# Kernel tuning notes

Hardware: AMD Instinct MI355X
Metric: run time of the kernel (lower is better)

Reference implementation:

```python
import jax, jax.numpy as jnp
import numpy as np

GRID_SIZE = 5
GRID_LO, GRID_HI = -1.0, 1.0


def setup_inputs() -> dict:
    key = jax.random.key(0)
    k1, k2 = jax.random.split(key)
    B, out_dim, in_dim, H, W = 8, 64, 64, 192, 192
    G = GRID_SIZE + 1
    x = jax.random.normal(k1, (B, in_dim, H, W), dtype=jnp.float32)
    coef = jax.random.normal(k2, (B, out_dim, in_dim, G), dtype=jnp.float32) * 0.1
    return {"x": x, "coef": coef}


def reference(x, coef):
    # x: [B, in_dim, H, W]; coef: [B, out_dim, in_dim, G] with G = grid_size + 1
    G = GRID_SIZE + 1
    grid = jnp.linspace(GRID_LO, GRID_HI, G, dtype=x.dtype)
    lo, hi = grid[0], grid[-1]
    spacing = grid[1] - grid[0]

    B, in_dim, H, W = x.shape
    out_dim = coef.shape[1]
    P = H * W

    xf = x.reshape(B, in_dim, P)
    xc = jnp.clip(xf, lo, hi)
    nx = (xc - lo) / spacing                      # normalized coordinate in [0, grid_size]
    idx = jnp.clip(jnp.floor(nx).astype(jnp.int32), 0, GRID_SIZE - 1)  # left knot
    frac = nx - idx.astype(x.dtype)               # fractional offset (grad flows via nx)
    w1 = 1.0 - frac
    w2 = frac
    idx_next = jnp.clip(idx + 1, 0, GRID_SIZE)    # right knot (max index = G-1)

    # Two-hot interpolation weights over the G grid points: [B, in, P, G]
    Wt = (w1[..., None] * jax.nn.one_hot(idx, G, dtype=x.dtype)
          + w2[..., None] * jax.nn.one_hot(idx_next, G, dtype=x.dtype))

    # result[b,o,p] = sum_i sum_g Wt[b,i,p,g] * coef[b,o,i,g]
    out = jnp.einsum('bipg,boig->bop', Wt, coef)
    return out.reshape(B, out_dim, H, W)
```

## Files before the change

kernel.cpp:

```cpp
#include <hip/hip_runtime.h>
#include <stdint.h>


typedef __fp16 half8_t __attribute__((ext_vector_type(8)));
typedef __fp16 half2_t __attribute__((ext_vector_type(2)));
typedef float f32x4 __attribute__((ext_vector_type(4)));

#define NBATCH 8
#define OD 64
#define ID 64
#define PIX 36864
#define NG 6
#define PT 192
#define KI 32
#define NCHUNK 2
#define KROW 384
#define PROW 196
#define PTILES (PIX / PT)

#define CPRE_BYTES (NBATCH * OD * KROW * 2)

__global__ __launch_bounds__(256)
void prep_coef(const float* __restrict__ coef, __fp16* __restrict__ cpre) {
  int idx = blockIdx.x * 256 + threadIdx.x;
  int b = idx / (OD * KROW);
  int rem = idx % (OD * KROW);
  int o = rem / KROW;
  int k = rem % KROW;
  int c = k / 192;
  int s = k % 192;
  int g = s >> 5;
  int iof = s & 31;
  float v = coef[((size_t)(b * OD + o) * ID + c * KI + iof) * NG + g];
  cpre[idx] = (__fp16)v;
}

__global__ __launch_bounds__(256, 3)
void kan_mfma2(const float* __restrict__ x, const __fp16* __restrict__ cpre,
               float* __restrict__ out) {
  const int t = threadIdx.x;
  const int lane = t & 63;
  const int wave = t >> 6;
  const int q8 = lane >> 4;
  const int col = lane & 15;

  const int bid = blockIdx.x;
  const int b = bid / PTILES;
  const int p0 = (bid % PTILES) * PT;

  __shared__ float nx_lds[KI][PROW] __attribute__((aligned(16)));

  f32x4 acc[4][3];
#pragma unroll
  for (int i = 0; i < 4; ++i)
#pragma unroll
    for (int j = 0; j < 3; ++j)
      acc[i][j] = (f32x4){0.f, 0.f, 0.f, 0.f};

  const float* xb = x + (size_t)b * ID * PIX + p0;
  const __fp16* caw = cpre + (size_t)b * OD * KROW + (size_t)col * KROW + q8 * 8;
  const int srow = t >> 3;
  const int pb = (t & 7) * 24;

  f32x4 xv[6];
#pragma unroll
  for (int j = 0; j < 6; ++j)
    xv[j] = *(const f32x4*)(xb + (size_t)srow * PIX + pb + 4 * j);

#pragma unroll
  for (int c = 0; c < NCHUNK; ++c) {
    if (c > 0) __syncthreads();

#pragma unroll
    for (int j = 0; j < 6; ++j) {
      f32x4 n;
#pragma unroll
      for (int r = 0; r < 4; ++r) {
        float v = fminf(fmaxf(xv[j][r], -1.f), 1.f);
        n[r] = (v + 1.f) * 2.5f;
      }
      *(f32x4*)&nx_lds[srow][pb + 4 * j] = n;
    }
    __syncthreads();

    if (c + 1 < NCHUNK) {
#pragma unroll
      for (int j = 0; j < 6; ++j)
        xv[j] = *(const f32x4*)(xb + (size_t)(KI + srow) * PIX + pb + 4 * j);
    }

    float nxv[3][8];
#pragma unroll
    for (int pti = 0; pti < 3; ++pti) {
      int p = wave * 48 + pti * 16 + col;
#pragma unroll
      for (int j = 0; j < 8; ++j)
        nxv[pti][j] = nx_lds[q8 * 8 + j][p];
    }

    const __fp16* cac = caw + c * 192;
#pragma unroll
    for (int ks = 0; ks < 6; ++ks) {
      half8_t af[4];
#pragma unroll
      for (int ot = 0; ot < 4; ++ot)
        af[ot] = *(const half8_t*)(cac + (size_t)(ot * 16) * KROW + ks * 32);

      const float gf = (float)ks;
#pragma unroll
      for (int pti = 0; pti < 3; ++pti) {
        union { half2_t h2[4]; half8_t v; } bu;
#pragma unroll
        for (int jj = 0; jj < 4; ++jj) {
          float h0 = fmaxf(0.f, 1.f - fabsf(nxv[pti][2 * jj] - gf));
          float h1 = fmaxf(0.f, 1.f - fabsf(nxv[pti][2 * jj + 1] - gf));
          bu.h2[jj] = __builtin_amdgcn_cvt_pkrtz(h0, h1);
        }
#pragma unroll
        for (int ot = 0; ot < 4; ++ot)
          acc[ot][pti] = __builtin_amdgcn_mfma_f32_16x16x32_f16(
              af[ot], bu.v, acc[ot][pti], 0, 0, 0);
      }
    }
  }

  float* ob = out + (size_t)b * OD * PIX + p0;
#pragma unroll
  for (int ot = 0; ot < 4; ++ot) {
#pragma unroll
    for (int pti = 0; pti < 3; ++pti) {
      int p = wave * 48 + pti * 16 + col;
#pragma unroll
      for (int r = 0; r < 4; ++r) {
        int o = ot * 16 + q8 * 4 + r;
        ob[(size_t)o * PIX + p] = acc[ot][pti][r];
      }
    }
  }
}

#define AROW 104
#define XROW 18
__global__ __launch_bounds__(256, 2)
void kan_mfma_fb(const float* __restrict__ x, const float* __restrict__ coef,
                 float* __restrict__ out) {
  const int t = threadIdx.x;
  const int lane = t & 63;
  const int wave = t >> 6;
  const int q8 = lane >> 4;
  const int col = lane & 15;
  const int bid = blockIdx.x;
  const int b = bid / PTILES;
  const int p0 = (bid % PTILES) * PT;

  __shared__ __fp16 A_lds[OD][AROW] __attribute__((aligned(16)));
  __shared__ float nxf[PT][XROW] __attribute__((aligned(16)));

  f32x4 acc[4][3];
#pragma unroll
  for (int i = 0; i < 4; ++i)
#pragma unroll
    for (int j = 0; j < 3; ++j) acc[i][j] = (f32x4){0.f, 0.f, 0.f, 0.f};

  const float* xb = x + (size_t)b * ID * PIX + p0;
  const float* cb = coef + (size_t)b * OD * ID * NG;
  const int iof0 = (q8 & 1) * 8;
  const int ghalf = q8 >> 1;

  for (int c = 0; c < 4; ++c) {
    const int i0 = c * 16;
    __syncthreads();
#pragma unroll
    for (int j = 0; j < 12; ++j) {
      int lin = j * 256 + t;
      int p = lin % PT;
      int iof = lin / PT;
      float xvv = xb[(size_t)(i0 + iof) * PIX + p];
      xvv = fminf(fmaxf(xvv, -1.f), 1.f);
      nxf[p][iof] = (xvv + 1.f) * 2.5f;
    }
    {
      const int o = t >> 2;
      const int r0 = (t & 3) * 24;
      const float* crow = cb + o * (ID * NG) + i0 * NG + r0;
#pragma unroll
      for (int j = 0; j < 24; ++j) {
        int r = r0 + j;
        int iof = r / 6;
        int g = r - iof * 6;
        A_lds[o][g * 16 + iof] = (__fp16)crow[j];
      }
    }
    __syncthreads();

    float nxv[3][8];
#pragma unroll
    for (int pti = 0; pti < 3; ++pti) {
      int p = wave * 48 + pti * 16 + col;
#pragma unroll
      for (int j = 0; j < 8; ++j) nxv[pti][j] = nxf[p][iof0 + j];
    }
#pragma unroll
    for (int ks = 0; ks < 3; ++ks) {
      half8_t af[4];
#pragma unroll
      for (int ot = 0; ot < 4; ++ot)
        af[ot] = *(const half8_t*)&A_lds[ot * 16 + col][ks * 32 + q8 * 8];
      const float gf = (float)(2 * ks + ghalf);
#pragma unroll
      for (int pti = 0; pti < 3; ++pti) {
        union { half2_t h2[4]; half8_t v; } bu;
#pragma unroll
        for (int jj = 0; jj < 4; ++jj) {
          float h0 = fmaxf(0.f, 1.f - fabsf(nxv[pti][2 * jj] - gf));
          float h1 = fmaxf(0.f, 1.f - fabsf(nxv[pti][2 * jj + 1] - gf));
          bu.h2[jj] = __builtin_amdgcn_cvt_pkrtz(h0, h1);
        }
#pragma unroll
        for (int ot = 0; ot < 4; ++ot)
          acc[ot][pti] = __builtin_amdgcn_mfma_f32_16x16x32_f16(
              af[ot], bu.v, acc[ot][pti], 0, 0, 0);
      }
    }
  }
  float* ob = out + (size_t)b * OD * PIX + p0;
#pragma unroll
  for (int ot = 0; ot < 4; ++ot)
#pragma unroll
    for (int pti = 0; pti < 3; ++pti) {
      int p = wave * 48 + pti * 16 + col;
#pragma unroll
      for (int r = 0; r < 4; ++r)
        ob[(size_t)(ot * 16 + q8 * 4 + r) * PIX + p] = acc[ot][pti][r];
    }
}

extern "C" void kernel_launch(void* const* d_in, const int* in_sizes, int n_in,
                              void* d_out, int out_size, void* d_ws, size_t ws_size,
                              hipStream_t stream) {
  const float* x = (const float*)d_in[0];
  const float* coef = (const float*)d_in[1];
  float* out = (float*)d_out;
  if (ws_size >= (size_t)CPRE_BYTES) {
    __fp16* cpre = (__fp16*)d_ws;
    hipLaunchKernelGGL(prep_coef, dim3((NBATCH * OD * KROW) / 256), dim3(256), 0,
                       stream, coef, cpre);
    hipLaunchKernelGGL(kan_mfma2, dim3(NBATCH * PTILES), dim3(256), 0, stream, x,
                       cpre, out);
  } else {
    hipLaunchKernelGGL(kan_mfma_fb, dim3(NBATCH * PTILES), dim3(256), 0, stream,
                       x, coef, out);
  }
}
```

Measured before the change: 159.7 us.

## Load x directly per wave, swap MFMA operands for vectorized output stores

Removes the LDS staging of normalized x and both block barriers; each lane now loads its x values straight from global memory in the pattern MFMA needs. The MFMA operands are swapped, so the two-hot weights become the A operand and the coefficients the B operand. This transposes the accumulator layout and allows 16-byte vector stores of the output instead of scalar stores. The occupancy hint rises from 3 to 4 blocks per CU. The trade-off is that x loads become strided scalar loads (16 lanes contiguous per row) without the earlier prefetch overlap.

Result: slower. 175.5 us (+10.0%).

```diff
diff --git a/kernel.cpp b/kernel.cpp
--- a/kernel.cpp
+++ b/kernel.cpp
@@ -15,7 +15,6 @@
 #define KI 32
 #define NCHUNK 2
 #define KROW 384
-#define PROW 196
 #define PTILES (PIX / PT)
 
 #define CPRE_BYTES (NBATCH * OD * KROW * 2)
@@ -35,8 +34,8 @@
   cpre[idx] = (__fp16)v;
 }
 
-__global__ __launch_bounds__(256, 3)
-void kan_mfma2(const float* __restrict__ x, const __fp16* __restrict__ cpre,
+__global__ __launch_bounds__(256, 4)
+void kan_mfma3(const float* __restrict__ x, const __fp16* __restrict__ cpre,
                float* __restrict__ out) {
   const int t = threadIdx.x;
   const int lane = t & 63;
@@ -44,11 +43,8 @@
   const int q8 = lane >> 4;
   const int col = lane & 15;
 
-  const int bid = blockIdx.x;
-  const int b = bid / PTILES;
-  const int p0 = (bid % PTILES) * PT;
-
-  __shared__ float nx_lds[KI][PROW] __attribute__((aligned(16)));
+  const int b = blockIdx.x / PTILES;
+  const int pw = (blockIdx.x % PTILES) * PT + wave * 48;
 
   f32x4 acc[4][3];
 #pragma unroll
@@ -57,86 +53,53 @@
     for (int j = 0; j < 3; ++j)
       acc[i][j] = (f32x4){0.f, 0.f, 0.f, 0.f};
 
-  const float* xb = x + (size_t)b * ID * PIX + p0;
-  const __fp16* caw = cpre + (size_t)b * OD * KROW + (size_t)col * KROW + q8 * 8;
-  const int srow = t >> 3;
-  const int pb = (t & 7) * 24;
-
-  f32x4 xv[6];
-#pragma unroll
-  for (int j = 0; j < 6; ++j)
-    xv[j] = *(const f32x4*)(xb + (size_t)srow * PIX + pb + 4 * j);
+  const float* xb = x + (size_t)b * ID * PIX + pw + col;
+  const __fp16* cb = cpre + (size_t)b * OD * KROW + q8 * 8;
 
 #pragma unroll
   for (int c = 0; c < NCHUNK; ++c) {
-    if (c > 0) __syncthreads();
-
-#pragma unroll
-    for (int j = 0; j < 6; ++j) {
-      f32x4 n;
-#pragma unroll
-      for (int r = 0; r < 4; ++r) {
-        float v = fminf(fmaxf(xv[j][r], -1.f), 1.f);
-        n[r] = (v + 1.f) * 2.5f;
-      }
-      *(f32x4*)&nx_lds[srow][pb + 4 * j] = n;
-    }
-    __syncthreads();
-
-    if (c + 1 < NCHUNK) {
-#pragma unroll
-      for (int j = 0; j < 6; ++j)
-        xv[j] = *(const f32x4*)(xb + (size_t)(KI + srow) * PIX + pb + 4 * j);
-    }
-
     float nxv[3][8];
 #pragma unroll
-    for (int pti = 0; pti < 3; ++pti) {
-      int p = wave * 48 + pti * 16 + col;
-#pragma unroll
-      for (int j = 0; j < 8; ++j)
-        nxv[pti][j] = nx_lds[q8 * 8 + j][p];
-    }
-
-    const __fp16* cac = caw + c * 192;
+    for (int pti = 0; pti < 3; ++pti)
+#pragma unroll
+      for (int j = 0; j < 8; ++j) {
+        float xv = xb[(size_t)(c * KI + q8 * 8 + j) * PIX + pti * 16];
+        xv = fminf(fmaxf(xv, -1.f), 1.f);
+        nxv[pti][j] = (xv + 1.f) * 2.5f;
+      }
+
+    const __fp16* cc = cb + c * 192;
 #pragma unroll
     for (int ks = 0; ks < 6; ++ks) {
-      half8_t af[4];
+      half8_t bf[4];
 #pragma unroll
       for (int ot = 0; ot < 4; ++ot)
-        af[ot] = *(const half8_t*)(cac + (size_t)(ot * 16) * KROW + ks * 32);
+        bf[ot] = *(const half8_t*)(cc + (size_t)(ot * 16 + col) * KROW + ks * 32);
 
       const float gf = (float)ks;
 #pragma unroll
       for (int pti = 0; pti < 3; ++pti) {
-        union { half2_t h2[4]; half8_t v; } bu;
+        union { half2_t h2[4]; half8_t v; } au;
 #pragma unroll
         for (int jj = 0; jj < 4; ++jj) {
           float h0 = fmaxf(0.f, 1.f - fabsf(nxv[pti][2 * jj] - gf));
           float h1 = fmaxf(0.f, 1.f - fabsf(nxv[pti][2 * jj + 1] - gf));
-          bu.h2[jj] = __builtin_amdgcn_cvt_pkrtz(h0, h1);
+          au.h2[jj] = __builtin_amdgcn_cvt_pkrtz(h0, h1);
         }
 #pragma unroll
         for (int ot = 0; ot < 4; ++ot)
           acc[ot][pti] = __builtin_amdgcn_mfma_f32_16x16x32_f16(
-              af[ot], bu.v, acc[ot][pti], 0, 0, 0);
+              au.v, bf[ot], acc[ot][pti], 0, 0, 0);
       }
     }
   }
 
-  float* ob = out + (size_t)b * OD * PIX + p0;
-#pragma unroll
-  for (int ot = 0; ot < 4; ++ot) {
-#pragma unroll
-    for (int pti = 0; pti < 3; ++pti) {
-      int p = wave * 48 + pti * 16 + col;
-#pragma unroll
-      for (int r = 0; r < 4; ++r) {
-        int o = ot * 16 + q8 * 4 + r;
-        ob[(size_t)o * PIX + p] = acc[ot][pti][r];
-      }
-    }
-  }
+  float* ob = out + (size_t)b * OD * PIX + pw + q8 * 4;
+#pragma unroll
+  for (int ot = 0; ot < 4; ++ot)
+#pragma unroll
+    for (int pti = 0; pti < 3; ++pti)
+      *(f32x4*)(ob + (size_t)(ot * 16 + col) * PIX + pti * 16) = acc[ot][pti];
 }
 
 #define AROW 104
@@ -245,7 +208,7 @@
     __fp16* cpre = (__fp16*)d_ws;
     hipLaunchKernelGGL(prep_coef, dim3((NBATCH * OD * KROW) / 256), dim3(256), 0,
                        stream, coef, cpre);
-    hipLaunchKernelGGL(kan_mfma2, dim3(NBATCH * PTILES), dim3(256), 0, stream, x,
+    hipLaunchKernelGGL(kan_mfma3, dim3(NBATCH * PTILES), dim3(256), 0, stream, x,
                        cpre, out);
   } else {
     hipLaunchKernelGGL(kan_mfma_fb, dim3(NBATCH * PTILES), dim3(256), 0, stream,
```
